# Performance work log

Measured on AMD Instinct MI355X. Metric: run time of the kernel, lower is better.

Reference implementation:

```python
import jax, jax.numpy as jnp
import numpy as np

DIM = 768
HEADS = 8

def setup_inputs() -> dict:
    key = jax.random.key(0)
    k1, k2, k3, k4 = jax.random.split(key, 4)
    x = jax.random.normal(k1, (4, 2048, DIM), dtype=jnp.float32)
    # torch Linear(D, 3D, bias=False): weight [3D, D]; store transposed [D, 3D]
    W_qkv = jax.random.normal(k2, (DIM, 3 * DIM), dtype=jnp.float32) * (DIM ** -0.5)
    W_o = jax.random.normal(k3, (DIM, DIM), dtype=jnp.float32) * (DIM ** -0.5)
    b_o = jax.random.normal(k4, (DIM,), dtype=jnp.float32) * 0.01
    return {"x": x, "W_qkv": W_qkv, "W_o": W_o, "b_o": b_o}

def reference(x, W_qkv, W_o, b_o):
    B, N, D = x.shape
    H = HEADS
    dh = D // H
    scale = dh ** -0.5
    qkv = x @ W_qkv                                   # [B, N, 3D]
    qkv = qkv.reshape(B, N, 3, H, dh)
    qkv = jnp.transpose(qkv, (2, 0, 3, 1, 4))         # [3, B, H, N, dh]
    Q, K, V = qkv[0], qkv[1], qkv[2]
    scores = jnp.einsum('bhqd,bhkd->bhqk', Q, K) * scale  # [B, H, N, N]
    attn = jax.nn.softmax(scores, axis=-1)
    out = jnp.einsum('bhqk,bhkd->bhqd', attn, V)      # [B, H, N, dh]
    # Faithful to original: reshape [B,H,N,dh] -> [B,N,D] WITHOUT head transpose
    out = out.reshape(B, N, D)
    return out @ W_o + b_o
```

## Files before the change

kernel.cpp:

```cpp
#include <hip/hip_runtime.h>

typedef __attribute__((ext_vector_type(8))) short short8;
typedef __attribute__((ext_vector_type(4))) float f32x4;
typedef __attribute__((ext_vector_type(4))) _Float16 half4;
typedef __attribute__((ext_vector_type(8))) _Float16 half8;
typedef __attribute__((ext_vector_type(2))) __fp16 fp16x2;

#define B_SZ 4
#define NSEQ 2048
#define DIM  768
#define NH   8
#define DH   96

__device__ __forceinline__ unsigned short f2bf(float f) {
  unsigned int u = __float_as_uint(f);
  u += 0x7fffu + ((u >> 16) & 1u);
  return (unsigned short)(u >> 16);
}

__device__ __forceinline__ float fexp2(float x) {
#if __has_builtin(__builtin_amdgcn_exp2f)
  return __builtin_amdgcn_exp2f(x);
#else
  return exp2f(x);
#endif
}

__device__ __forceinline__ void glds16(const void* g, void* l) {
  __builtin_amdgcn_global_load_lds((const __attribute__((address_space(1))) void*)g,
                                   (__attribute__((address_space(3))) void*)l, 16, 0, 0);
}

__global__ __launch_bounds__(256) void prep_kernel(
    const float* __restrict__ x, unsigned short* __restrict__ xb,
    const float* __restrict__ Wqkv, unsigned short* __restrict__ wqkvT,
    const float* __restrict__ Wo, unsigned short* __restrict__ woT)
{
  int blk = blockIdx.x;
  if (blk < 6144) {
    int i = blk * 256 + threadIdx.x;
    float4 v = ((const float4*)x)[i];
    ushort4 o;
    o.x = f2bf(v.x); o.y = f2bf(v.y); o.z = f2bf(v.z); o.w = f2bf(v.w);
    ((ushort4*)xb)[i] = o;
    return;
  }
  __shared__ float tile[32][33];
  const float* W; unsigned short* WT; int ncols, bx, by;
  if (blk < 7872) { int r = blk - 6144; W = Wqkv; WT = wqkvT; ncols = 2304; bx = r % 72; by = r / 72; }
  else            { int r = blk - 7872; W = Wo;   WT = woT;   ncols = 768;  bx = r % 24; by = r / 24; }
  int tx = threadIdx.x & 31, ty = threadIdx.x >> 5;
  int c0 = bx * 32, r0 = by * 32;
#pragma unroll
  for (int i = 0; i < 4; i++)
    tile[ty + i * 8][tx] = W[(size_t)(r0 + ty + i * 8) * ncols + c0 + tx];
  __syncthreads();
#pragma unroll
  for (int i = 0; i < 4; i++)
    WT[(size_t)(c0 + ty + i * 8) * 768 + r0 + tx] = f2bf(tile[tx][ty + i * 8]);
}

template <int EPI>
__global__ __launch_bounds__(256) void gemm_bt(
    const unsigned short* __restrict__ A, const unsigned short* __restrict__ Bt,
    unsigned short* __restrict__ qo, unsigned short* __restrict__ ko,
    _Float16* __restrict__ vo, float* __restrict__ fo,
    const float* __restrict__ bias)
{
  __shared__ unsigned short As[128 * 64];
  __shared__ unsigned short Bs[128 * 64];
  const int t = threadIdx.x;
  const int w = t >> 6, lane = t & 63;
  const int l15 = lane & 15, qd = lane >> 4;
  const int rsw = l15 & 7;
  const int m0 = blockIdx.y * 128, n0 = blockIdx.x * 128;
  const int wm = (w >> 1) * 64, wn = (w & 1) * 64;

  int off[2];
#pragma unroll
  for (int j = 0; j < 2; j++) {
    int cl = j * 64 + lane;
    int r16 = cl >> 3, c = cl & 7;
    off[j] = r16 * DIM + ((c ^ (r16 & 7)) * 8);
  }
  const unsigned short* ga = A  + (size_t)(m0 + w * 16) * DIM;
  const unsigned short* gb = Bt + (size_t)(n0 + w * 16) * DIM;

  f32x4 acc[4][4] = {};

  for (int k0 = 0; k0 < DIM; k0 += 64) {
#pragma unroll
    for (int j = 0; j < 2; j++) {
      glds16(ga + k0 + off[j],            &As[w * 1024 + j * 512]);
      glds16(ga + 64 * DIM + k0 + off[j], &As[4096 + w * 1024 + j * 512]);
      glds16(gb + k0 + off[j],            &Bs[w * 1024 + j * 512]);
      glds16(gb + 64 * DIM + k0 + off[j], &Bs[4096 + w * 1024 + j * 512]);
    }
    __syncthreads();
#pragma unroll
    for (int ks = 0; ks < 2; ks++) {
      short8 af[4], bfr[4];
#pragma unroll
      for (int i = 0; i < 4; i++)
        af[i]  = *(const short8*)&As[(wm + i * 16 + l15) * 64 + (((ks * 4 + qd) ^ rsw)) * 8];
#pragma unroll
      for (int i = 0; i < 4; i++)
        bfr[i] = *(const short8*)&Bs[(wn + i * 16 + l15) * 64 + (((ks * 4 + qd) ^ rsw)) * 8];
#pragma unroll
      for (int mi = 0; mi < 4; mi++)
#pragma unroll
        for (int ni = 0; ni < 4; ni++)
          acc[mi][ni] = __builtin_amdgcn_mfma_f32_16x16x32_bf16(af[mi], bfr[ni], acc[mi][ni], 0, 0, 0);
    }
    __syncthreads();
  }

#pragma unroll
  for (int mi = 0; mi < 4; mi++)
#pragma unroll
    for (int ni = 0; ni < 4; ni++) {
      int rowb = m0 + wm + mi * 16 + qd * 4;
      int col  = n0 + wn + ni * 16 + l15;
      if (EPI == 0) {
        int b = rowb >> 11, n = rowb & 2047;
        int s = col / DIM;
        int rem = col - s * DIM;
        int hh = rem / DH;
        int c = rem - hh * DH;
        size_t bh = (size_t)(b * NH + hh);
        if (s == 2) {
          half4 pk;
#pragma unroll
          for (int r = 0; r < 4; r++) pk[r] = (_Float16)acc[mi][ni][r];
          *(half4*)&vo[(bh * DH + c) * NSEQ + n] = pk;
        } else if (s == 0) {
#pragma unroll
          for (int r = 0; r < 4; r++)
            qo[(bh * NSEQ + n + r) * DH + c] = f2bf(acc[mi][ni][r] * 0.1472444679f);
        } else {
#pragma unroll
          for (int r = 0; r < 4; r++)
            ko[(bh * NSEQ + n + r) * DH + c] = f2bf(acc[mi][ni][r]);
        }
      } else {
#pragma unroll
        for (int r = 0; r < 4; r++)
          fo[(size_t)(rowb + r) * DIM + col] = acc[mi][ni][r] + bias[col];
      }
    }
}

__global__ __launch_bounds__(256, 2) void flash_kernel(
    const unsigned short* __restrict__ Qb, const unsigned short* __restrict__ Kb,
    const _Float16* __restrict__ Vtb, unsigned short* __restrict__ Z)
{
  __shared__ unsigned char smem[49152];

  const int t = threadIdx.x, w = t >> 6, lane = t & 63;
  const int l15 = lane & 15, qd = lane >> 4;
  const int swz = (l15 >> 1) & 3;
  const int vswz = l15 & 7;

  const int bid = blockIdx.x;
  const int h  = bid & 7;
  const int qt = (bid >> 3) & 15;
  const int b  = bid >> 7;

  const size_t bh = (size_t)(b * NH + h);
  const unsigned short* Qg = Qb + (bh * NSEQ + (size_t)qt * 128) * DH;
  const unsigned short* Kg = Kb + bh * NSEQ * DH;
  const _Float16*       Vg = Vtb + bh * (size_t)DH * NSEQ;

  int qoff[6];
#pragma unroll
  for (int i = 0; i < 6; i++) {
    int L = i * 256 + t;
    int r = L / 12, c = L - r * 12;
    qoff[i] = r * 96 + ((c ^ ((r >> 1) & 3)) * 8);
  }
  int koff[3];
#pragma unroll
  for (int i = 0; i < 3; i++) {
    int L = w * 192 + i * 64 + lane;
    int r = L / 12, c = L - r * 12;
    int fk = r >> 4, m = r & 15;
    int key = 32 * (fk & 1) + 4 * (fk >> 1) + 8 * (m >> 2) + (m & 3);
    koff[i] = key * 96 + ((c ^ ((r >> 1) & 3)) * 8);
  }
  int voff[3];
#pragma unroll
  for (int i = 0; i < 3; i++) {
    int L = i * 256 + t;
    int r = L >> 3, c = L & 7;
    voff[i] = r * NSEQ + ((c ^ (r & 7)) * 8);
  }

  short8 qa[2][3];
  f32x4 o[2][7] = {};
  const half8 onef = {(_Float16)1.f, (_Float16)1.f, (_Float16)1.f, (_Float16)1.f,
                      (_Float16)1.f, (_Float16)1.f, (_Float16)1.f, (_Float16)1.f};

  auto stageKV = [&](int kt, int bufoff) {
    unsigned short* Kd = (unsigned short*)(smem + bufoff);
    _Float16*       Vd = (_Float16*)(smem + bufoff + 12288);
    const unsigned short* Kt = Kg + (size_t)kt * 64 * DH;
#pragma unroll
    for (int i = 0; i < 3; i++)
      glds16(Kt + koff[i], &Kd[w * 1536 + i * 512]);
    const _Float16* Vt = Vg + kt * 64;
#pragma unroll
    for (int i = 0; i < 3; i++)
      glds16(Vt + voff[i], &Vd[(i * 256 + w * 64) * 8]);
  };

  auto compute = [&](int bufoff) {
    const unsigned short* Ks = (const unsigned short*)(smem + bufoff);
    const _Float16*       Vs = (const _Float16*)(smem + bufoff + 12288);

    f32x4 s[2][4] = {};
    __builtin_amdgcn_s_setprio(1);
#pragma unroll
    for (int ks = 0; ks < 3; ks++)
#pragma unroll
      for (int fk = 0; fk < 4; fk++) {
        short8 kf = *(const short8*)&Ks[(fk * 16 + l15) * 96 + ((ks * 4 + qd) ^ swz) * 8];
        s[0][fk] = __builtin_amdgcn_mfma_f32_16x16x32_bf16(kf, qa[0][ks], s[0][fk], 0, 0, 0);
        s[1][fk] = __builtin_amdgcn_mfma_f32_16x16x32_bf16(kf, qa[1][ks], s[1][fk], 0, 0, 0);
      }
    __builtin_amdgcn_s_setprio(0);

    half4 pf2[2][4];
#pragma unroll
    for (int fq = 0; fq < 2; fq++)
#pragma unroll
      for (int fk = 0; fk < 4; fk++) {
        union { fp16x2 h2[2]; half4 h4; } u;
        u.h2[0] = __builtin_amdgcn_cvt_pkrtz(fexp2(s[fq][fk][0] - 12.f), fexp2(s[fq][fk][1] - 12.f));
        u.h2[1] = __builtin_amdgcn_cvt_pkrtz(fexp2(s[fq][fk][2] - 12.f), fexp2(s[fq][fk][3] - 12.f));
        pf2[fq][fk] = u.h4;
      }

#pragma unroll
    for (int pp = 0; pp < 2; pp++) {
      union { half4 h4[2]; half8 h8; } bu0, bu1;
      bu0.h4[0] = pf2[0][pp]; bu0.h4[1] = pf2[0][pp + 2];
      bu1.h4[0] = pf2[1][pp]; bu1.h4[1] = pf2[1][pp + 2];
      __builtin_amdgcn_s_setprio(1);
#pragma unroll
      for (int fc = 0; fc < 6; fc++) {
        half8 vf = *(const half8*)&Vs[(fc * 16 + l15) * 64 + ((pp * 4 + qd) ^ vswz) * 8];
        o[0][fc] = __builtin_amdgcn_mfma_f32_16x16x32_f16(vf, bu0.h8, o[0][fc], 0, 0, 0);
        o[1][fc] = __builtin_amdgcn_mfma_f32_16x16x32_f16(vf, bu1.h8, o[1][fc], 0, 0, 0);
      }
      o[0][6] = __builtin_amdgcn_mfma_f32_16x16x32_f16(onef, bu0.h8, o[0][6], 0, 0, 0);
      o[1][6] = __builtin_amdgcn_mfma_f32_16x16x32_f16(onef, bu1.h8, o[1][6], 0, 0, 0);
      __builtin_amdgcn_s_setprio(0);
    }
  };

#pragma unroll
  for (int i = 0; i < 6; i++)
    glds16(Qg + qoff[i], &((unsigned short*)smem)[i * 2048 + w * 512]);
  stageKV(0, 24576);
  __syncthreads();

  const unsigned short* Qs = (const unsigned short*)smem;
#pragma unroll
  for (int fq = 0; fq < 2; fq++)
#pragma unroll
    for (int ks = 0; ks < 3; ks++)
      qa[fq][ks] = *(const short8*)&Qs[(w * 32 + fq * 16 + l15) * 96 + ((ks * 4 + qd) ^ swz) * 8];
  __syncthreads();

  for (int kt = 0; kt < 32; kt += 2) {
    stageKV(kt + 1, 0);
    compute(24576);
    __syncthreads();
    if (kt < 30) stageKV(kt + 2, 24576);
    compute(0);
    __syncthreads();
  }

#pragma unroll
  for (int fq = 0; fq < 2; fq++) {
    float inv = 1.0f / o[fq][6][0];
    int q = qt * 128 + w * 32 + fq * 16 + l15;
    size_t zbase = ((size_t)b * NSEQ + h * 256 + (q >> 3)) * DIM + (q & 7) * DH;
#pragma unroll
    for (int fc = 0; fc < 6; fc++)
#pragma unroll
      for (int r = 0; r < 4; r += 2) {
        unsigned int pkd = (unsigned int)f2bf(o[fq][fc][r] * inv)
                         | ((unsigned int)f2bf(o[fq][fc][r + 1] * inv) << 16);
        *(unsigned int*)&Z[zbase + fc * 16 + qd * 4 + r] = pkd;
      }
  }
}

extern "C" void kernel_launch(void* const* d_in, const int* in_sizes, int n_in,
                              void* d_out, int out_size, void* d_ws, size_t ws_size,
                              hipStream_t stream)
{
  (void)in_sizes; (void)n_in; (void)out_size; (void)ws_size;
  const float* x    = (const float*)d_in[0];
  const float* Wqkv = (const float*)d_in[1];
  const float* Wo   = (const float*)d_in[2];
  const float* bo   = (const float*)d_in[3];
  float* out = (float*)d_out;

  unsigned short* ws    = (unsigned short*)d_ws;
  unsigned short* xb    = ws;
  unsigned short* wqkvT = xb    + (size_t)8192 * 768;
  unsigned short* woT   = wqkvT + (size_t)2304 * 768;
  unsigned short* Qw    = woT   + (size_t)768 * 768;
  unsigned short* Kw    = Qw    + (size_t)6291456;
  _Float16*       Vw    = (_Float16*)(Kw + (size_t)6291456);
  unsigned short* Zw    = (unsigned short*)(Vw + (size_t)6291456);

  prep_kernel<<<8448, 256, 0, stream>>>(x, xb, Wqkv, wqkvT, Wo, woT);
  gemm_bt<0><<<dim3(18, 64), 256, 0, stream>>>(xb, wqkvT, Qw, Kw, Vw, nullptr, nullptr);
  flash_kernel<<<512, 256, 0, stream>>>(Qw, Kw, Vw, Zw);
  gemm_bt<1><<<dim3(6, 64), 256, 0, stream>>>(Zw, woT, nullptr, nullptr, nullptr, out, bo);
}
```

Baseline: 207.7 us.

## Fuse all stages into one persistent kernel with software grid barriers

Replaces the four separate launches (prep, QKV GEMM, flash attention, output GEMM) with a single persistent kernel of 512 blocks that loops over each stage's work and separates stages with an atomic-counter grid barrier. The aim is to remove launch gaps and tail idle time between kernels. It relies on all 512 blocks being co-resident (two per CU) and adds a memset plus barrier spin cost. The GEMM stages also lose parallelism, since 1152 QKV tiles now run as strided loops over 512 blocks and the output GEMM uses only 384 blocks. The old multi-kernel path is kept as a fallback when the workspace is too small.

Measured after the change: 681.6 us. +228.2%, slower.

```diff
diff --git a/kernel.cpp b/kernel.cpp
--- a/kernel.cpp
+++ b/kernel.cpp
@@ -6,7 +6,6 @@
 typedef __attribute__((ext_vector_type(8))) _Float16 half8;
 typedef __attribute__((ext_vector_type(2))) __fp16 fp16x2;
 
-#define B_SZ 4
 #define NSEQ 2048
 #define DIM  768
 #define NH   8
@@ -31,49 +30,65 @@
                                    (__attribute__((address_space(3))) void*)l, 16, 0, 0);
 }
 
-__global__ __launch_bounds__(256) void prep_kernel(
-    const float* __restrict__ x, unsigned short* __restrict__ xb,
-    const float* __restrict__ Wqkv, unsigned short* __restrict__ wqkvT,
-    const float* __restrict__ Wo, unsigned short* __restrict__ woT)
-{
-  int blk = blockIdx.x;
-  if (blk < 6144) {
-    int i = blk * 256 + threadIdx.x;
-    float4 v = ((const float4*)x)[i];
-    ushort4 o;
-    o.x = f2bf(v.x); o.y = f2bf(v.y); o.z = f2bf(v.z); o.w = f2bf(v.w);
-    ((ushort4*)xb)[i] = o;
-    return;
-  }
-  __shared__ float tile[32][33];
+__device__ __forceinline__ void gridbar(unsigned int* sync, unsigned int target) {
+  __threadfence();
+  __syncthreads();
+  if (threadIdx.x == 0) {
+    __hip_atomic_fetch_add(sync, 1u, __ATOMIC_RELEASE, __HIP_MEMORY_SCOPE_AGENT);
+    unsigned int cap = 0;
+    while (__hip_atomic_load(sync, __ATOMIC_ACQUIRE, __HIP_MEMORY_SCOPE_AGENT) < target
+           && cap < (4u << 20)) { __builtin_amdgcn_s_sleep(8); ++cap; }
+  }
+  __syncthreads();
+  __threadfence();
+}
+
+
+__device__ __forceinline__ void prep_cvt_job(int j, const float* __restrict__ x,
+                                             unsigned short* __restrict__ xb) {
+  int i = j * 256 + threadIdx.x;
+  float4 v = ((const float4*)x)[i];
+  ushort4 o;
+  o.x = f2bf(v.x); o.y = f2bf(v.y); o.z = f2bf(v.z); o.w = f2bf(v.w);
+  ((ushort4*)xb)[i] = o;
+}
+
+__device__ __forceinline__ void prep_wt_job(int r, const float* __restrict__ Wqkv,
+                                            unsigned short* __restrict__ wqkvT,
+                                            const float* __restrict__ Wo,
+                                            unsigned short* __restrict__ woT,
+                                            unsigned char* smem) {
+  float* tile = (float*)smem;
   const float* W; unsigned short* WT; int ncols, bx, by;
-  if (blk < 7872) { int r = blk - 6144; W = Wqkv; WT = wqkvT; ncols = 2304; bx = r % 72; by = r / 72; }
-  else            { int r = blk - 7872; W = Wo;   WT = woT;   ncols = 768;  bx = r % 24; by = r / 24; }
+  if (r < 1728) { W = Wqkv; WT = wqkvT; ncols = 2304; bx = r % 72; by = r / 72; }
+  else          { int q = r - 1728; W = Wo; WT = woT; ncols = 768; bx = q % 24; by = q / 24; }
   int tx = threadIdx.x & 31, ty = threadIdx.x >> 5;
   int c0 = bx * 32, r0 = by * 32;
 #pragma unroll
   for (int i = 0; i < 4; i++)
-    tile[ty + i * 8][tx] = W[(size_t)(r0 + ty + i * 8) * ncols + c0 + tx];
+    tile[(ty + i * 8) * 33 + tx] = W[(size_t)(r0 + ty + i * 8) * ncols + c0 + tx];
   __syncthreads();
 #pragma unroll
   for (int i = 0; i < 4; i++)
-    WT[(size_t)(c0 + ty + i * 8) * 768 + r0 + tx] = f2bf(tile[tx][ty + i * 8]);
+    WT[(size_t)(c0 + ty + i * 8) * 768 + r0 + tx] = f2bf(tile[tx * 33 + ty + i * 8]);
+  __syncthreads();
 }
 
 template <int EPI>
-__global__ __launch_bounds__(256) void gemm_bt(
+__device__ __forceinline__ void gemm_tile(
+    int bx, int by,
     const unsigned short* __restrict__ A, const unsigned short* __restrict__ Bt,
     unsigned short* __restrict__ qo, unsigned short* __restrict__ ko,
     _Float16* __restrict__ vo, float* __restrict__ fo,
-    const float* __restrict__ bias)
-{
-  __shared__ unsigned short As[128 * 64];
-  __shared__ unsigned short Bs[128 * 64];
+    const float* __restrict__ bias, unsigned char* smem)
+{
+  unsigned short* As = (unsigned short*)smem;
+  unsigned short* Bs = (unsigned short*)(smem + 16384);
   const int t = threadIdx.x;
   const int w = t >> 6, lane = t & 63;
   const int l15 = lane & 15, qd = lane >> 4;
   const int rsw = l15 & 7;
-  const int m0 = blockIdx.y * 128, n0 = blockIdx.x * 128;
+  const int m0 = by * 128, n0 = bx * 128;
   const int wm = (w >> 1) * 64, wn = (w & 1) * 64;
 
   int off[2];
@@ -150,18 +165,15 @@
     }
 }
 
-__global__ __launch_bounds__(256, 2) void flash_kernel(
-    const unsigned short* __restrict__ Qb, const unsigned short* __restrict__ Kb,
-    const _Float16* __restrict__ Vtb, unsigned short* __restrict__ Z)
-{
-  __shared__ unsigned char smem[49152];
-
+__device__ __forceinline__ void flash_block(
+    int bid, const unsigned short* __restrict__ Qb, const unsigned short* __restrict__ Kb,
+    const _Float16* __restrict__ Vtb, unsigned short* __restrict__ Z, unsigned char* smem)
+{
   const int t = threadIdx.x, w = t >> 6, lane = t & 63;
   const int l15 = lane & 15, qd = lane >> 4;
   const int swz = (l15 >> 1) & 3;
   const int vswz = l15 & 7;
 
-  const int bid = blockIdx.x;
   const int h  = bid & 7;
   const int qt = (bid >> 3) & 15;
   const int b  = bid >> 7;
@@ -297,11 +309,69 @@
   }
 }
 
+
+__global__ __launch_bounds__(256, 2) void mega_kernel(
+    const float* __restrict__ x, const float* __restrict__ Wqkv,
+    const float* __restrict__ Wo, const float* __restrict__ bo,
+    unsigned short* __restrict__ xb, unsigned short* __restrict__ wqkvT,
+    unsigned short* __restrict__ woT, unsigned short* __restrict__ Qw,
+    unsigned short* __restrict__ Kw, _Float16* __restrict__ Vw,
+    unsigned short* __restrict__ Zw, float* __restrict__ out,
+    unsigned int* __restrict__ sync)
+{
+  __shared__ unsigned char smem[49152];
+  const int bid = blockIdx.x;
+
+  for (int j = bid; j < 6144; j += 512) prep_cvt_job(j, x, xb);
+  for (int j = bid; j < 2304; j += 512) prep_wt_job(j, Wqkv, wqkvT, Wo, woT, smem);
+  gridbar(sync, 512);
+
+  for (int j = bid; j < 1152; j += 512)
+    gemm_tile<0>(j % 18, j / 18, xb, wqkvT, Qw, Kw, Vw, nullptr, nullptr, smem);
+  gridbar(sync, 1024);
+
+  flash_block(bid, Qw, Kw, Vw, Zw, smem);
+  gridbar(sync, 1536);
+
+  if (bid < 384)
+    gemm_tile<1>(bid % 6, bid / 6, Zw, woT, nullptr, nullptr, nullptr, out, bo, smem);
+}
+
+__global__ __launch_bounds__(256) void prep_kernel(
+    const float* __restrict__ x, unsigned short* __restrict__ xb,
+    const float* __restrict__ Wqkv, unsigned short* __restrict__ wqkvT,
+    const float* __restrict__ Wo, unsigned short* __restrict__ woT)
+{
+  __shared__ unsigned char smem[4224];
+  int blk = blockIdx.x;
+  if (blk < 6144) { prep_cvt_job(blk, x, xb); return; }
+  prep_wt_job(blk - 6144, Wqkv, wqkvT, Wo, woT, smem);
+}
+
+template <int EPI>
+__global__ __launch_bounds__(256) void gemm_bt(
+    const unsigned short* __restrict__ A, const unsigned short* __restrict__ Bt,
+    unsigned short* __restrict__ qo, unsigned short* __restrict__ ko,
+    _Float16* __restrict__ vo, float* __restrict__ fo,
+    const float* __restrict__ bias)
+{
+  __shared__ unsigned char smem[32768];
+  gemm_tile<EPI>(blockIdx.x, blockIdx.y, A, Bt, qo, ko, vo, fo, bias, smem);
+}
+
+__global__ __launch_bounds__(256, 2) void flash_kernel(
+    const unsigned short* __restrict__ Qb, const unsigned short* __restrict__ Kb,
+    const _Float16* __restrict__ Vtb, unsigned short* __restrict__ Z)
+{
+  __shared__ unsigned char smem[49152];
+  flash_block(blockIdx.x, Qb, Kb, Vtb, Z, smem);
+}
+
 extern "C" void kernel_launch(void* const* d_in, const int* in_sizes, int n_in,
                               void* d_out, int out_size, void* d_ws, size_t ws_size,
                               hipStream_t stream)
 {
-  (void)in_sizes; (void)n_in; (void)out_size; (void)ws_size;
+  (void)in_sizes; (void)n_in; (void)out_size;
   const float* x    = (const float*)d_in[0];
   const float* Wqkv = (const float*)d_in[1];
   const float* Wo   = (const float*)d_in[2];
@@ -317,8 +387,16 @@
   _Float16*       Vw    = (_Float16*)(Kw + (size_t)6291456);
   unsigned short* Zw    = (unsigned short*)(Vw + (size_t)6291456);
 
-  prep_kernel<<<8448, 256, 0, stream>>>(x, xb, Wqkv, wqkvT, Wo, woT);
-  gemm_bt<0><<<dim3(18, 64), 256, 0, stream>>>(xb, wqkvT, Qw, Kw, Vw, nullptr, nullptr);
-  flash_kernel<<<512, 256, 0, stream>>>(Qw, Kw, Vw, Zw);
-  gemm_bt<1><<<dim3(6, 64), 256, 0, stream>>>(Zw, woT, nullptr, nullptr, nullptr, out, bo);
-}
+  const size_t base = 67633152;
+  if (ws_size >= base + 64) {
+    unsigned int* sync = (unsigned int*)((char*)d_ws + base);
+    hipMemsetAsync(sync, 0, 64, stream);
+    mega_kernel<<<512, 256, 0, stream>>>(x, Wqkv, Wo, bo, xb, wqkvT, woT,
+                                         Qw, Kw, Vw, Zw, out, sync);
+  } else {
+    prep_kernel<<<8448, 256, 0, stream>>>(x, xb, Wqkv, wqkvT, Wo, woT);
+    gemm_bt<0><<<dim3(18, 64), 256, 0, stream>>>(xb, wqkvT, Qw, Kw, Vw, nullptr, nullptr);
+    flash_kernel<<<512, 256, 0, stream>>>(Qw, Kw, Vw, Zw);
+    gemm_bt<1><<<dim3(6, 64), 256, 0, stream>>>(Zw, woT, nullptr, nullptr, nullptr, out, bo);
+  }
+}
```
